# Performance work log

Hardware: AMD Instinct MI355X
Metric: run time of the kernel (lower is better)

## Reference

```python
import jax, jax.numpy as jnp
import numpy as np

F_DIM = 128        # feature_dim
LATENT = 256       # latent_dim
HEADS = 4          # n_head
N_GRAPHS = 256
NODES_PER = 100    # < 180 (pos table size)
N = N_GRAPHS * NODES_PER
DEG = 8
E = N * DEG
MAX_POS = 180
NEG_SLOPE = 0.2


def sinusoid_table(n_node, d):
    pos = np.arange(n_node, dtype=np.float64)[:, None]
    j = np.arange(d, dtype=np.float64)[None, :]
    ang = pos / np.power(10000.0, 2.0 * (np.floor(j / 2.0)) / d)
    ang[:, 0::2] = np.sin(ang[:, 0::2])
    ang[:, 1::2] = np.cos(ang[:, 1::2])
    return jnp.asarray(ang, dtype=jnp.float32)  # [n_node, d]


def gat_layer(x, src, dst, W, a_src, a_dst, bias):
    # x: [N, in], W: [in, H*C], a_src/a_dst: [H, C], bias: [H*C]
    H, C = a_src.shape
    xl = (x @ W).reshape(N, H, C)                      # [N,H,C]
    s = jnp.einsum('nhc,hc->nh', xl, a_src)            # [N,H]
    d = jnp.einsum('nhc,hc->nh', xl, a_dst)            # [N,H]
    e = jax.nn.leaky_relu(s[src] + d[dst], NEG_SLOPE)  # [E,H]
    emax = jax.ops.segment_max(e, dst, num_segments=N)
    ex = jnp.exp(e - emax[dst])
    den = jax.ops.segment_sum(ex, dst, num_segments=N)
    alpha = ex / (den[dst] + 1e-16)                    # [E,H]
    out = jax.ops.segment_sum(alpha[:, :, None] * xl[src], dst, num_segments=N)
    return out.reshape(N, H * C) + bias


def setup_inputs() -> dict:
    key = jax.random.key(0)
    ks = jax.random.split(key, 20)
    sc = 0.05
    z = jax.random.normal(ks[0], (N_GRAPHS, LATENT), dtype=jnp.float32)
    batch = jnp.repeat(jnp.arange(N_GRAPHS, dtype=jnp.int64), NODES_PER)
    base = (jnp.arange(N, dtype=jnp.int64) // NODES_PER) * NODES_PER
    nbr = jax.random.randint(ks[1], (N, DEG), 0, NODES_PER, dtype=jnp.int64)
    src = (base[:, None] + nbr).reshape(-1)
    dst = jnp.repeat(jnp.arange(N, dtype=jnp.int64), DEG)
    edge_index = jnp.stack([src, dst], 0)
    HF = HEADS * F_DIM
    p = {
        'W0': jax.random.normal(ks[2], (LATENT, F_DIM)) * sc,
        'b0': jnp.zeros((F_DIM,), jnp.float32),
        'W1': jax.random.normal(ks[3], (2 * F_DIM, HF)) * sc,
        'as1': jax.random.normal(ks[4], (HEADS, F_DIM)) * sc,
        'ad1': jax.random.normal(ks[5], (HEADS, F_DIM)) * sc,
        'b1': jnp.zeros((HF,), jnp.float32),
        'W2': jax.random.normal(ks[6], (HF, HF)) * sc,
        'as2': jax.random.normal(ks[7], (HEADS, F_DIM)) * sc,
        'ad2': jax.random.normal(ks[8], (HEADS, F_DIM)) * sc,
        'b2': jnp.zeros((HF,), jnp.float32),
        'W3': jax.random.normal(ks[9], (HF, HF)) * sc,
        'as3': jax.random.normal(ks[10], (HEADS, F_DIM)) * sc,
        'ad3': jax.random.normal(ks[11], (HEADS, F_DIM)) * sc,
        'b3': jnp.zeros((HF,), jnp.float32),
        'Wg': jax.random.normal(ks[12], (HF, F_DIM)) * sc,
        'bg': jnp.zeros((F_DIM,), jnp.float32),
        'Wf': jax.random.normal(ks[13], (F_DIM, 5)) * sc,
        'bf': jnp.zeros((5,), jnp.float32),
    }
    return {'z': z, 'edge_index': edge_index, 'batch': batch, **p}


def reference(z, edge_index, batch, W0, b0, W1, as1, ad1, b1,
              W2, as2, ad2, b2, W3, as3, ad3, b3, Wg, bg, Wf, bf):
    # node order within each graph (intended semantics of node_order_within_batch)
    counts = jax.ops.segment_sum(jnp.ones((N,), jnp.int32), batch, num_segments=N_GRAPHS)
    cum = jnp.concatenate([jnp.zeros((1,), jnp.int32), jnp.cumsum(counts)[:-1]])
    order = jnp.arange(N, dtype=jnp.int32) - cum[batch]
    pos = sinusoid_table(MAX_POS, F_DIM)[order]        # [N, F]  (detached buffer)

    h = (z @ W0 + b0)[batch]                           # [N, F]
    h = jax.nn.relu(jnp.concatenate([h, pos], axis=1)) # [N, 2F]

    # PyG GATConv default add_self_loops=True
    loop = jnp.arange(N, dtype=edge_index.dtype)
    src = jnp.concatenate([edge_index[0], loop])
    dst = jnp.concatenate([edge_index[1], loop])

    h = jax.nn.relu(gat_layer(h, src, dst, W1, as1, ad1, b1))
    h = jax.nn.relu(gat_layer(h, src, dst, W2, as2, ad2, b2))
    h = jax.nn.relu(gat_layer(h, src, dst, W3, as3, ad3, b3))
    h = jax.nn.relu(h @ Wg + bg)
    return h @ Wf + bf                                 # [N, 5]
```

## Files before the change

### kernel.cpp

```cpp
#include <hip/hip_runtime.h>
#include <hip/hip_bf16.h>
#include <math.h>

#define N_GRAPHS 256
#define NODES_PER 100
#define NN (N_GRAPHS * NODES_PER)
#define DEG 8
#define FD 128
#define LAT 256
#define HFD 512
#define MAXPOS 180
#define NEG_SLOPE 0.2f

typedef _Float16 half8 __attribute__((ext_vector_type(8)));
typedef float float4v __attribute__((ext_vector_type(4)));

__device__ __forceinline__ int xcd_swz(int bid, int total) {
    int q = total >> 3;
    return (bid & 7) * q + (bid >> 3);
}

__global__ void sintab_kernel(float* __restrict__ tab) {
    int p = blockIdx.x;
    int j = threadIdx.x;
    double ang = (double)p / pow(10000.0, (double)(2 * (j / 2)) / 128.0);
    double v = (j & 1) ? cos(ang) : sin(ang);
    tab[p * FD + j] = (float)v;
}

__global__ void g0_kernel(const float* __restrict__ z, const float* __restrict__ W0,
                          const float* __restrict__ b0, float* __restrict__ g0) {
    __shared__ float s_z[LAT];
    int g = blockIdx.x;
    int j = threadIdx.x;
    s_z[j]       = z[g * LAT + j];
    s_z[j + 128] = z[g * LAT + 128 + j];
    __syncthreads();
    float acc = 0.f;
    #pragma unroll 8
    for (int k = 0; k < LAT; ++k)
        acc += s_z[k] * W0[k * FD + j];
    g0[g * FD + j] = acc + b0[j];
}

__global__ void build_x1_kernel(const float* __restrict__ g0, const float* __restrict__ tab,
                                const int* __restrict__ batch, _Float16* __restrict__ x1) {
    __shared__ int s_b, s_ord;
    int i = blockIdx.x;
    int t = threadIdx.x;
    if (t == 0) {
        int b = batch[i];
        int lo = 0, hi = i;
        while (lo < hi) { int mid = (lo + hi) >> 1; if (batch[mid] < b) lo = mid + 1; else hi = mid; }
        s_b = b;
        s_ord = i - lo;
    }
    __syncthreads();
    float v = (t < 128) ? g0[s_b * FD + t] : tab[s_ord * FD + (t - 128)];
    x1[(size_t)i * 256 + t] = (_Float16)fmaxf(v, 0.f);
}

__global__ void wconv_kernel(const float* __restrict__ in, _Float16* __restrict__ out,
                             int K, int Nw) {
    __shared__ float tile[32][33];
    int kb = blockIdx.y * 32, nb = blockIdx.x * 32;
    int tx = threadIdx.x & 31, ty = threadIdx.x >> 5;
    #pragma unroll
    for (int r = 0; r < 4; ++r)
        tile[ty + 8 * r][tx] = in[(size_t)(kb + ty + 8 * r) * Nw + nb + tx];
    __syncthreads();
    #pragma unroll
    for (int r = 0; r < 4; ++r)
        out[(size_t)(nb + ty + 8 * r) * K + kb + tx] = (_Float16)tile[tx][ty + 8 * r];
}

template <int MODE>
__global__ __launch_bounds__(256) void hgemm_kernel(
    const _Float16* __restrict__ X,
    const _Float16* __restrict__ Wt,
    const float* __restrict__ bias,
    void* __restrict__ Yv,
    int K, int ldy, int nbx) {
    __shared__ __align__(16) _Float16 As[2][128 * 32];
    __shared__ __align__(16) _Float16 Bs[2][128 * 32];
    const int lin = xcd_swz(blockIdx.x, gridDim.x);
    const int row0 = (lin / nbx) * 128;
    const int col0 = (lin % nbx) * 128;
    const int tid  = threadIdx.x;
    const int lane = tid & 63;
    const int wave = tid >> 6;
    const int wm = wave >> 1;
    const int wn = wave & 1;

    const int sr = tid >> 1;
    const int sq = (tid & 1) * 2;
    const size_t ga = (size_t)(row0 + sr) * K + sq * 8;
    const size_t gb = (size_t)(col0 + sr) * K + sq * 8;
    const int ss = (sr >> 1) & 3;
    const int w0 = sr * 32 + ((sq ^ ss) * 8);
    const int w1 = sr * 32 + (((sq + 1) ^ ss) * 8);

    const int kq  = lane >> 4;
    const int l15 = lane & 15;

    float4v acc[4][4];
    #pragma unroll
    for (int i = 0; i < 4; ++i)
        #pragma unroll
        for (int j = 0; j < 4; ++j)
            acc[i][j] = (float4v){0.f, 0.f, 0.f, 0.f};

    half8 ra0, ra1, rb0, rb1;
    ra0 = *(const half8*)&X[ga];      ra1 = *(const half8*)&X[ga + 8];
    rb0 = *(const half8*)&Wt[gb];     rb1 = *(const half8*)&Wt[gb + 8];
    *(half8*)&As[0][w0] = ra0;  *(half8*)&As[0][w1] = ra1;
    *(half8*)&Bs[0][w0] = rb0;  *(half8*)&Bs[0][w1] = rb1;

    const int nk = K >> 5;
    for (int ks = 0; ks < nk; ++ks) {
        __syncthreads();
        const int cur = ks & 1;
        if (ks + 1 < nk) {
            int kb = (ks + 1) << 5;
            ra0 = *(const half8*)&X[ga + kb];   ra1 = *(const half8*)&X[ga + kb + 8];
            rb0 = *(const half8*)&Wt[gb + kb];  rb1 = *(const half8*)&Wt[gb + kb + 8];
        }
        half8 af[4], bf[4];
        #pragma unroll
        for (int mi = 0; mi < 4; ++mi) {
            int r = wm * 64 + mi * 16 + l15;
            af[mi] = *(const half8*)&As[cur][r * 32 + ((kq ^ ((r >> 1) & 3)) * 8)];
        }
        #pragma unroll
        for (int ni = 0; ni < 4; ++ni) {
            int c = wn * 64 + ni * 16 + l15;
            bf[ni] = *(const half8*)&Bs[cur][c * 32 + ((kq ^ ((c >> 1) & 3)) * 8)];
        }
        #pragma unroll
        for (int mi = 0; mi < 4; ++mi)
            #pragma unroll
            for (int ni = 0; ni < 4; ++ni)
                acc[mi][ni] = __builtin_amdgcn_mfma_f32_16x16x32_f16(af[mi], bf[ni], acc[mi][ni], 0, 0, 0);
        if (ks + 1 < nk) {
            const int nxt = cur ^ 1;
            *(half8*)&As[nxt][w0] = ra0;  *(half8*)&As[nxt][w1] = ra1;
            *(half8*)&Bs[nxt][w0] = rb0;  *(half8*)&Bs[nxt][w1] = rb1;
        }
    }

    #pragma unroll
    for (int mi = 0; mi < 4; ++mi) {
        int r = row0 + wm * 64 + mi * 16 + ((lane >> 4) << 2);
        #pragma unroll
        for (int ni = 0; ni < 4; ++ni) {
            int c = col0 + wn * 64 + ni * 16 + l15;
            #pragma unroll
            for (int j = 0; j < 4; ++j) {
                float v = acc[mi][ni][j];
                if (MODE == 1) {
                    v += bias[c]; v = fmaxf(v, 0.f);
                    ((float*)Yv)[(size_t)(r + j) * ldy + c] = v;
                } else {
                    ((_Float16*)Yv)[(size_t)(r + j) * ldy + c] = (_Float16)v;
                }
            }
        }
    }
}

__global__ void sd_kernel(const _Float16* __restrict__ xl,
                          const float* __restrict__ a_src, const float* __restrict__ a_dst,
                          float* __restrict__ s, float* __restrict__ d) {
    int wave = threadIdx.x >> 6;
    int lane = threadIdx.x & 63;
    int n = blockIdx.x * 4 + wave;
    int h = lane >> 4;
    int c0 = (lane & 15) * 8;
    half8 x = *(const half8*)&xl[(size_t)n * HFD + h * FD + c0];
    float4v a0 = *(const float4v*)&a_src[h * FD + c0];
    float4v a1 = *(const float4v*)&a_src[h * FD + c0 + 4];
    float4v e0 = *(const float4v*)&a_dst[h * FD + c0];
    float4v e1 = *(const float4v*)&a_dst[h * FD + c0 + 4];
    float ps = 0.f, pd = 0.f;
    #pragma unroll
    for (int j = 0; j < 4; ++j) {
        ps += (float)x[j] * a0[j] + (float)x[j + 4] * a1[j];
        pd += (float)x[j] * e0[j] + (float)x[j + 4] * e1[j];
    }
    #pragma unroll
    for (int m = 8; m >= 1; m >>= 1) {
        ps += __shfl_xor(ps, m);
        pd += __shfl_xor(pd, m);
    }
    if ((lane & 15) == 0) { s[n * 4 + h] = ps; d[n * 4 + h] = pd; }
}

__global__ void agg_kernel(const _Float16* __restrict__ xl,
                           const float* __restrict__ s, const float* __restrict__ d,
                           const int* __restrict__ esrc,
                           const float* __restrict__ bias,
                           _Float16* __restrict__ xout) {
    int wave = threadIdx.x >> 6;
    int lane = threadIdx.x & 63;
    int blk = xcd_swz(blockIdx.x, gridDim.x);
    int i = blk * 4 + wave;
    int h = lane >> 4;

    int sk = (lane < 8) ? esrc[i * DEG + lane] : i;
    int srcs[9];
    #pragma unroll
    for (int k = 0; k < 9; ++k) srcs[k] = __shfl(sk, k);

    float dh = d[i * 4 + h];
    float e[9];
    float m = -1e30f;
    #pragma unroll
    for (int k = 0; k < 9; ++k) {
        float v = s[srcs[k] * 4 + h] + dh;
        v = (v >= 0.f) ? v : NEG_SLOPE * v;
        e[k] = v;
        m = fmaxf(m, v);
    }
    float den = 0.f;
    #pragma unroll
    for (int k = 0; k < 9; ++k) { e[k] = __expf(e[k] - m); den += e[k]; }
    float inv = 1.f / (den + 1e-16f);

    int c0 = lane * 8;
    float acc[8] = {};
    #pragma unroll
    for (int k = 0; k < 9; ++k) {
        half8 x = *(const half8*)&xl[(size_t)srcs[k] * HFD + c0];
        float a = e[k] * inv;
        #pragma unroll
        for (int j = 0; j < 8; ++j) acc[j] += a * (float)x[j];
    }
    float4v b0 = *(const float4v*)&bias[c0];
    float4v b1 = *(const float4v*)&bias[c0 + 4];
    half8 o;
    #pragma unroll
    for (int j = 0; j < 4; ++j) {
        o[j]     = (_Float16)fmaxf(acc[j] + b0[j], 0.f);
        o[j + 4] = (_Float16)fmaxf(acc[j + 4] + b1[j], 0.f);
    }
    *(half8*)&xout[(size_t)i * HFD + c0] = o;
}

__global__ void out_kernel(const float* __restrict__ H, const float* __restrict__ Wf,
                           const float* __restrict__ bfv, float* __restrict__ out) {
    int wave = threadIdx.x >> 6;
    int lane = threadIdx.x & 63;
    int n = blockIdx.x * 4 + wave;
    float v0 = H[(size_t)n * FD + lane];
    float v1 = H[(size_t)n * FD + 64 + lane];
    #pragma unroll
    for (int q = 0; q < 5; ++q) {
        float p = v0 * Wf[lane * 5 + q] + v1 * Wf[(lane + 64) * 5 + q];
        #pragma unroll
        for (int m = 32; m >= 1; m >>= 1) p += __shfl_xor(p, m);
        if (lane == 0) out[n * 5 + q] = p + bfv[q];
    }
}

extern "C" void kernel_launch(void* const* d_in, const int* in_sizes, int n_in,
                              void* d_out, int out_size, void* d_ws, size_t ws_size,
                              hipStream_t stream) {
    const float* z    = (const float*)d_in[0];
    const int*  eidx  = (const int*)d_in[1];
    const int*  batch = (const int*)d_in[2];
    const float* W0  = (const float*)d_in[3];
    const float* b0  = (const float*)d_in[4];
    const float* W1  = (const float*)d_in[5];
    const float* as1 = (const float*)d_in[6];
    const float* ad1 = (const float*)d_in[7];
    const float* b1  = (const float*)d_in[8];
    const float* W2  = (const float*)d_in[9];
    const float* as2 = (const float*)d_in[10];
    const float* ad2 = (const float*)d_in[11];
    const float* b2  = (const float*)d_in[12];
    const float* W3  = (const float*)d_in[13];
    const float* as3 = (const float*)d_in[14];
    const float* ad3 = (const float*)d_in[15];
    const float* b3  = (const float*)d_in[16];
    const float* Wg  = (const float*)d_in[17];
    const float* bg  = (const float*)d_in[18];
    const float* Wf  = (const float*)d_in[19];
    const float* bfv = (const float*)d_in[20];
    float* out = (float*)d_out;

    float* ws   = (float*)d_ws;
    float* tab  = ws;
    float* g0   = tab + 23040;
    float* sbuf = g0 + 32768;
    float* dbuf = sbuf + (size_t)NN * 4;
    float* Hbuf = dbuf + (size_t)NN * 4;
    _Float16* Yh  = (_Float16*)(Hbuf + (size_t)NN * 128);
    _Float16* Xh  = Yh + (size_t)NN * 512;
    _Float16* W1t = Xh + (size_t)NN * 512;
    _Float16* W2t = W1t + 512 * 256;
    _Float16* W3t = W2t + 512 * 512;
    _Float16* Wgt = W3t + 512 * 512;

    sintab_kernel<<<MAXPOS, FD, 0, stream>>>(tab);
    g0_kernel<<<N_GRAPHS, FD, 0, stream>>>(z, W0, b0, g0);
    build_x1_kernel<<<NN, 256, 0, stream>>>(g0, tab, batch, Xh);

    wconv_kernel<<<dim3(512 / 32, 256 / 32), 256, 0, stream>>>(W1, W1t, 256, 512);
    wconv_kernel<<<dim3(512 / 32, 512 / 32), 256, 0, stream>>>(W2, W2t, 512, 512);
    wconv_kernel<<<dim3(512 / 32, 512 / 32), 256, 0, stream>>>(W3, W3t, 512, 512);
    wconv_kernel<<<dim3(128 / 32, 512 / 32), 256, 0, stream>>>(Wg, Wgt, 512, 128);

    const int nbL = (NN / 128) * (HFD / 128);
    const int nbH = (NN / 128) * (FD / 128);

    hgemm_kernel<0><<<nbL, 256, 0, stream>>>(Xh, W1t, nullptr, Yh, 256, HFD, HFD / 128);
    sd_kernel<<<NN / 4, 256, 0, stream>>>(Yh, as1, ad1, sbuf, dbuf);
    agg_kernel<<<NN / 4, 256, 0, stream>>>(Yh, sbuf, dbuf, eidx, b1, Xh);

    hgemm_kernel<0><<<nbL, 256, 0, stream>>>(Xh, W2t, nullptr, Yh, 512, HFD, HFD / 128);
    sd_kernel<<<NN / 4, 256, 0, stream>>>(Yh, as2, ad2, sbuf, dbuf);
    agg_kernel<<<NN / 4, 256, 0, stream>>>(Yh, sbuf, dbuf, eidx, b2, Xh);

    hgemm_kernel<0><<<nbL, 256, 0, stream>>>(Xh, W3t, nullptr, Yh, 512, HFD, HFD / 128);
    sd_kernel<<<NN / 4, 256, 0, stream>>>(Yh, as3, ad3, sbuf, dbuf);
    agg_kernel<<<NN / 4, 256, 0, stream>>>(Yh, sbuf, dbuf, eidx, b3, Xh);

    hgemm_kernel<1><<<nbH, 256, 0, stream>>>(Xh, Wgt, bg, Hbuf, 512, FD, FD / 128);

    out_kernel<<<NN / 4, 256, 0, stream>>>(Hbuf, Wf, bfv, out);
}
```

Before: 302.8 us.

## Fuse attention-score and output-projection epilogues into GEMMs, merge weight conversions

The per-head attention dot products (s,d) are now computed in the GEMM epilogue: the 128-column tile is exactly one head, so each tile reduces across lanes, combines the two wave-halves through shared memory, and writes sbuf/dbuf. This removes the separate sd_kernel and its re-read of Yh. The final MODE 1 GEMM now applies bias and ReLU and multiplies by Wf in its epilogue, which removes Hbuf and out_kernel. The four weight-conversion launches become one. The cost is a larger epilogue with shuffles, an extra shared buffer, and a block-wide barrier in each GEMM.

```diff
diff --git a/kernel.cpp b/kernel.cpp
--- a/kernel.cpp
+++ b/kernel.cpp
@@ -60,10 +60,19 @@
     x1[(size_t)i * 256 + t] = (_Float16)fmaxf(v, 0.f);
 }
 
-__global__ void wconv_kernel(const float* __restrict__ in, _Float16* __restrict__ out,
-                             int K, int Nw) {
+__global__ void wconv_all_kernel(const float* __restrict__ W1, const float* __restrict__ W2,
+                                 const float* __restrict__ W3, const float* __restrict__ Wg,
+                                 _Float16* __restrict__ W1t, _Float16* __restrict__ W2t,
+                                 _Float16* __restrict__ W3t, _Float16* __restrict__ Wgt) {
     __shared__ float tile[32][33];
-    int kb = blockIdx.y * 32, nb = blockIdx.x * 32;
+    int b = blockIdx.x;
+    const float* in; _Float16* out; int K, Nw, tid2;
+    if (b < 128)      { in = W1; out = W1t; K = 256; Nw = 512; tid2 = b; }
+    else if (b < 384) { in = W2; out = W2t; K = 512; Nw = 512; tid2 = b - 128; }
+    else if (b < 640) { in = W3; out = W3t; K = 512; Nw = 512; tid2 = b - 384; }
+    else              { in = Wg; out = Wgt; K = 512; Nw = 128; tid2 = b - 640; }
+    int nxt = Nw / 32;
+    int nb = (tid2 % nxt) * 32, kb = (tid2 / nxt) * 32;
     int tx = threadIdx.x & 31, ty = threadIdx.x >> 5;
     #pragma unroll
     for (int r = 0; r < 4; ++r)
@@ -79,10 +88,17 @@
     const _Float16* __restrict__ X,
     const _Float16* __restrict__ Wt,
     const float* __restrict__ bias,
+    const float* __restrict__ a_src,
+    const float* __restrict__ a_dst,
+    float* __restrict__ sbuf,
+    float* __restrict__ dbuf,
+    const float* __restrict__ Wf,
+    const float* __restrict__ bfv,
     void* __restrict__ Yv,
     int K, int ldy, int nbx) {
     __shared__ __align__(16) _Float16 As[2][128 * 32];
     __shared__ __align__(16) _Float16 Bs[2][128 * 32];
+    __shared__ float red[5][128][2];
     const int lin = xcd_swz(blockIdx.x, gridDim.x);
     const int row0 = (lin / nbx) * 128;
     const int col0 = (lin % nbx) * 128;
@@ -142,57 +158,89 @@
             for (int ni = 0; ni < 4; ++ni)
                 acc[mi][ni] = __builtin_amdgcn_mfma_f32_16x16x32_f16(af[mi], bf[ni], acc[mi][ni], 0, 0, 0);
         if (ks + 1 < nk) {
-            const int nxt = cur ^ 1;
-            *(half8*)&As[nxt][w0] = ra0;  *(half8*)&As[nxt][w1] = ra1;
-            *(half8*)&Bs[nxt][w0] = rb0;  *(half8*)&Bs[nxt][w1] = rb1;
-        }
-    }
-
-    #pragma unroll
-    for (int mi = 0; mi < 4; ++mi) {
-        int r = row0 + wm * 64 + mi * 16 + ((lane >> 4) << 2);
+            const int nxt2 = cur ^ 1;
+            *(half8*)&As[nxt2][w0] = ra0;  *(half8*)&As[nxt2][w1] = ra1;
+            *(half8*)&Bs[nxt2][w0] = rb0;  *(half8*)&Bs[nxt2][w1] = rb1;
+        }
+    }
+
+    if (MODE == 0) {
+        const int h = col0 >> 7;
+        float asv[4], adv[4];
         #pragma unroll
         for (int ni = 0; ni < 4; ++ni) {
-            int c = col0 + wn * 64 + ni * 16 + l15;
+            int ch = wn * 64 + ni * 16 + l15;
+            asv[ni] = a_src[h * FD + ch];
+            adv[ni] = a_dst[h * FD + ch];
+        }
+        #pragma unroll
+        for (int mi = 0; mi < 4; ++mi) {
+            int rb = row0 + wm * 64 + mi * 16 + ((lane >> 4) << 2);
             #pragma unroll
             for (int j = 0; j < 4; ++j) {
-                float v = acc[mi][ni][j];
-                if (MODE == 1) {
-                    v += bias[c]; v = fmaxf(v, 0.f);
-                    ((float*)Yv)[(size_t)(r + j) * ldy + c] = v;
-                } else {
-                    ((_Float16*)Yv)[(size_t)(r + j) * ldy + c] = (_Float16)v;
+                float ps = 0.f, pd = 0.f;
+                #pragma unroll
+                for (int ni = 0; ni < 4; ++ni) {
+                    float v = acc[mi][ni][j];
+                    int c = col0 + wn * 64 + ni * 16 + l15;
+                    ((_Float16*)Yv)[(size_t)(rb + j) * ldy + c] = (_Float16)v;
+                    ps += v * asv[ni];
+                    pd += v * adv[ni];
+                }
+                #pragma unroll
+                for (int m = 8; m >= 1; m >>= 1) {
+                    ps += __shfl_xor(ps, m);
+                    pd += __shfl_xor(pd, m);
+                }
+                if (l15 == 0) {
+                    int rloc = wm * 64 + mi * 16 + ((lane >> 4) << 2) + j;
+                    red[0][rloc][wn] = ps;
+                    red[1][rloc][wn] = pd;
                 }
             }
         }
-    }
-}
-
-__global__ void sd_kernel(const _Float16* __restrict__ xl,
-                          const float* __restrict__ a_src, const float* __restrict__ a_dst,
-                          float* __restrict__ s, float* __restrict__ d) {
-    int wave = threadIdx.x >> 6;
-    int lane = threadIdx.x & 63;
-    int n = blockIdx.x * 4 + wave;
-    int h = lane >> 4;
-    int c0 = (lane & 15) * 8;
-    half8 x = *(const half8*)&xl[(size_t)n * HFD + h * FD + c0];
-    float4v a0 = *(const float4v*)&a_src[h * FD + c0];
-    float4v a1 = *(const float4v*)&a_src[h * FD + c0 + 4];
-    float4v e0 = *(const float4v*)&a_dst[h * FD + c0];
-    float4v e1 = *(const float4v*)&a_dst[h * FD + c0 + 4];
-    float ps = 0.f, pd = 0.f;
-    #pragma unroll
-    for (int j = 0; j < 4; ++j) {
-        ps += (float)x[j] * a0[j] + (float)x[j + 4] * a1[j];
-        pd += (float)x[j] * e0[j] + (float)x[j + 4] * e1[j];
-    }
-    #pragma unroll
-    for (int m = 8; m >= 1; m >>= 1) {
-        ps += __shfl_xor(ps, m);
-        pd += __shfl_xor(pd, m);
-    }
-    if ((lane & 15) == 0) { s[n * 4 + h] = ps; d[n * 4 + h] = pd; }
+        __syncthreads();
+        if (tid < 128) {
+            sbuf[(size_t)(row0 + tid) * 4 + h] = red[0][tid][0] + red[0][tid][1];
+            dbuf[(size_t)(row0 + tid) * 4 + h] = red[1][tid][0] + red[1][tid][1];
+        }
+    } else {
+        float bgv[4], wf[4][5];
+        #pragma unroll
+        for (int ni = 0; ni < 4; ++ni) {
+            int c = wn * 64 + ni * 16 + l15;
+            bgv[ni] = bias[c];
+            #pragma unroll
+            for (int q = 0; q < 5; ++q) wf[ni][q] = Wf[c * 5 + q];
+        }
+        #pragma unroll
+        for (int mi = 0; mi < 4; ++mi) {
+            #pragma unroll
+            for (int j = 0; j < 4; ++j) {
+                float vr[4];
+                #pragma unroll
+                for (int ni = 0; ni < 4; ++ni)
+                    vr[ni] = fmaxf(acc[mi][ni][j] + bgv[ni], 0.f);
+                #pragma unroll
+                for (int q = 0; q < 5; ++q) {
+                    float p = vr[0] * wf[0][q] + vr[1] * wf[1][q] + vr[2] * wf[2][q] + vr[3] * wf[3][q];
+                    #pragma unroll
+                    for (int m = 8; m >= 1; m >>= 1) p += __shfl_xor(p, m);
+                    if (l15 == 0) {
+                        int rloc = wm * 64 + mi * 16 + ((lane >> 4) << 2) + j;
+                        red[q][rloc][wn] = p;
+                    }
+                }
+            }
+        }
+        __syncthreads();
+        if (tid < 128) {
+            float* o = (float*)Yv;
+            #pragma unroll
+            for (int q = 0; q < 5; ++q)
+                o[(size_t)(row0 + tid) * 5 + q] = red[q][tid][0] + red[q][tid][1] + bfv[q];
+        }
+    }
 }
 
 __global__ void agg_kernel(const _Float16* __restrict__ xl,
@@ -244,22 +292,6 @@
         o[j + 4] = (_Float16)fmaxf(acc[j + 4] + b1[j], 0.f);
     }
     *(half8*)&xout[(size_t)i * HFD + c0] = o;
-}
-
-__global__ void out_kernel(const float* __restrict__ H, const float* __restrict__ Wf,
-                           const float* __restrict__ bfv, float* __restrict__ out) {
-    int wave = threadIdx.x >> 6;
-    int lane = threadIdx.x & 63;
-    int n = blockIdx.x * 4 + wave;
-    float v0 = H[(size_t)n * FD + lane];
-    float v1 = H[(size_t)n * FD + 64 + lane];
-    #pragma unroll
-    for (int q = 0; q < 5; ++q) {
-        float p = v0 * Wf[lane * 5 + q] + v1 * Wf[(lane + 64) * 5 + q];
-        #pragma unroll
-        for (int m = 32; m >= 1; m >>= 1) p += __shfl_xor(p, m);
-        if (lane == 0) out[n * 5 + q] = p + bfv[q];
-    }
 }
 
 extern "C" void kernel_launch(void* const* d_in, const int* in_sizes, int n_in,
@@ -293,8 +325,7 @@
     float* g0   = tab + 23040;
     float* sbuf = g0 + 32768;
     float* dbuf = sbuf + (size_t)NN * 4;
-    float* Hbuf = dbuf + (size_t)NN * 4;
-    _Float16* Yh  = (_Float16*)(Hbuf + (size_t)NN * 128);
+    _Float16* Yh  = (_Float16*)(dbuf + (size_t)NN * 4);
     _Float16* Xh  = Yh + (size_t)NN * 512;
     _Float16* W1t = Xh + (size_t)NN * 512;
     _Float16* W2t = W1t + 512 * 256;
@@ -304,28 +335,19 @@
     sintab_kernel<<<MAXPOS, FD, 0, stream>>>(tab);
     g0_kernel<<<N_GRAPHS, FD, 0, stream>>>(z, W0, b0, g0);
     build_x1_kernel<<<NN, 256, 0, stream>>>(g0, tab, batch, Xh);
-
-    wconv_kernel<<<dim3(512 / 32, 256 / 32), 256, 0, stream>>>(W1, W1t, 256, 512);
-    wconv_kernel<<<dim3(512 / 32, 512 / 32), 256, 0, stream>>>(W2, W2t, 512, 512);
-    wconv_kernel<<<dim3(512 / 32, 512 / 32), 256, 0, stream>>>(W3, W3t, 512, 512);
-    wconv_kernel<<<dim3(128 / 32, 512 / 32), 256, 0, stream>>>(Wg, Wgt, 512, 128);
+    wconv_all_kernel<<<704, 256, 0, stream>>>(W1, W2, W3, Wg, W1t, W2t, W3t, Wgt);
 
     const int nbL = (NN / 128) * (HFD / 128);
     const int nbH = (NN / 128) * (FD / 128);
 
-    hgemm_kernel<0><<<nbL, 256, 0, stream>>>(Xh, W1t, nullptr, Yh, 256, HFD, HFD / 128);
-    sd_kernel<<<NN / 4, 256, 0, stream>>>(Yh, as1, ad1, sbuf, dbuf);
+    hgemm_kernel<0><<<nbL, 256, 0, stream>>>(Xh, W1t, nullptr, as1, ad1, sbuf, dbuf, nullptr, nullptr, Yh, 256, HFD, HFD / 128);
     agg_kernel<<<NN / 4, 256, 0, stream>>>(Yh, sbuf, dbuf, eidx, b1, Xh);
 
-    hgemm_kernel<0><<<nbL, 256, 0, stream>>>(Xh, W2t, nullptr, Yh, 512, HFD, HFD / 128);
-    sd_kernel<<<NN / 4, 256, 0, stream>>>(Yh, as2, ad2, sbuf, dbuf);
+    hgemm_kernel<0><<<nbL, 256, 0, stream>>>(Xh, W2t, nullptr, as2, ad2, sbuf, dbuf, nullptr, nullptr, Yh, 512, HFD, HFD / 128);
     agg_kernel<<<NN / 4, 256, 0, stream>>>(Yh, sbuf, dbuf, eidx, b2, Xh);
 
-    hgemm_kernel<0><<<nbL, 256, 0, stream>>>(Xh, W3t, nullptr, Yh, 512, HFD, HFD / 128);
-    sd_kernel<<<NN / 4, 256, 0, stream>>>(Yh, as3, ad3, sbuf, dbuf);
+    hgemm_kernel<0><<<nbL, 256, 0, stream>>>(Xh, W3t, nullptr, as3, ad3, sbuf, dbuf, nullptr, nullptr, Yh, 512, HFD, HFD / 128);
     agg_kernel<<<NN / 4, 256, 0, stream>>>(Yh, sbuf, dbuf, eidx, b3, Xh);
 
-    hgemm_kernel<1><<<nbH, 256, 0, stream>>>(Xh, Wgt, bg, Hbuf, 512, FD, FD / 128);
-
-    out_kernel<<<NN / 4, 256, 0, stream>>>(Hbuf, Wf, bfv, out);
-}
+    hgemm_kernel<1><<<nbH, 256, 0, stream>>>(Xh, Wgt, bg, nullptr, nullptr, nullptr, nullptr, Wf, bfv, out, 512, 5, FD / 128);
+}
```

Result: faster. 294.3 us (-2.8%).
